# Kernel tuning notes

Hardware: AMD Instinct MI355X
Metric: run time of the kernel (lower is better)

## Reference

```python
import jax, jax.numpy as jnp
import numpy as np

B, E, H, NY, NX = 16, 128, 4, 32, 32


def setup_inputs() -> dict:
    key = jax.random.key(0)
    ks = jax.random.split(key, 7)
    w = lambda k, shape: jax.random.normal(k, shape, jnp.float32) * 0.02
    return {
        "x": jax.random.normal(ks[0], (B, E, NY, NX), jnp.float32),
        "Wk": w(ks[1], (E, E)), "bk": jnp.zeros((E,), jnp.float32),
        "Wq": w(ks[2], (E, E)), "bq": jnp.zeros((E,), jnp.float32),
        "Wv": w(ks[3], (E, E)), "bv": jnp.zeros((E,), jnp.float32),
        "Wu": w(ks[4], (E, E)), "bu": jnp.zeros((E,), jnp.float32),
        "pos_enc": w(ks[5], (H, (2 * NY - 1) * (2 * NX - 1))),
    }


def _conv1x1(x, W, b):
    # 1x1 conv == channel-mixing linear: (B,C,y,x) -> (B,O,y,x)
    return jnp.einsum('bcyx,oc->boyx', x, W) + b[None, :, None, None]


def _rel_indices(ny, nx):
    y = jnp.arange(ny)
    x = jnp.arange(nx)
    y1, x1, y2, x2 = jnp.meshgrid(y, x, y, x, indexing='ij')
    idx = (y1 - y2 + ny - 1) * (2 * nx - 1) + (x1 - x2 + nx - 1)
    return idx.reshape(ny * nx, ny * nx)  # (N, N)


def reference(x, Wk, bk, Wq, bq, Wv, bv, Wu, bu, pos_enc):
    b, e, ny, nx = x.shape
    h = pos_enc.shape[0]
    hc = e // h
    n = ny * nx
    scale = hc ** (-0.5)

    keys = _conv1x1(x, Wk, bk).reshape(b, h, hc, n)
    queries = _conv1x1(x, Wq, bq).reshape(b, h, hc, n)
    values = _conv1x1(x, Wv, bv).reshape(b, h, hc, n)

    # att[b,h,k,q] = sum_c keys[b,h,c,k] * queries[b,h,c,q]
    att = jnp.einsum('bhck,bhcq->bhkq', keys, queries) * scale

    # gathered relative position bias: (H, N, N)
    idx = _rel_indices(ny, nx)
    rel = pos_enc[:, idx]
    att = att + rel[None]

    # softmax over the key axis (dim=-2), as in the original
    att = jax.nn.softmax(att, axis=-2)

    out = jnp.einsum('bhck,bhkq->bhcq', values, att).reshape(b, e, ny, nx)
    return _conv1x1(out, Wu, bu)
```

## Files before the change

kernel.cpp:

```cpp
#include <hip/hip_runtime.h>
#include <hip/hip_bf16.h>

#define BN 16
#define EN 128
#define HN 4
#define HCN 32
#define NN 1024
#define POSN 3969

typedef short short8 __attribute__((ext_vector_type(8)));
typedef float f32x4 __attribute__((ext_vector_type(4)));

#define MFMA16(a, b, c) __builtin_amdgcn_mfma_f32_16x16x32_bf16((a), (b), (c), 0, 0, 0)

union Frag {
  short8 s8;
  uint2 u2[2];
  unsigned int u[4];
  unsigned short us[8];
};

__device__ __forceinline__ unsigned short bfbits(float x) {
  union { __hip_bfloat16 h; unsigned short u; } c;
  c.h = __float2bfloat16(x);
  return c.u;
}

__device__ __forceinline__ unsigned int pk2(float lo, float hi) {
  union { __hip_bfloat162 h2; unsigned int u; } c;
  c.h2 = __float22bfloat162_rn(make_float2(lo, hi));
  return c.u;
}

__device__ __forceinline__ void load_lds16(const void* g, void* l) {
  __builtin_amdgcn_global_load_lds(
      (const __attribute__((address_space(1))) void*)g,
      (__attribute__((address_space(3))) void*)l, 16, 0, 0);
}

__global__ __launch_bounds__(256) void qkv_prep_kernel(
    const float* __restrict__ x,
    const float* __restrict__ Wk, const float* __restrict__ bk, __hip_bfloat16* __restrict__ kb,
    const float* __restrict__ Wq, const float* __restrict__ bq, __hip_bfloat16* __restrict__ qb,
    const float* __restrict__ Wv, const float* __restrict__ bv, __hip_bfloat16* __restrict__ vb,
    const float* __restrict__ Wu, const float* __restrict__ pos,
    unsigned short* __restrict__ bias, Frag* __restrict__ whitab, Frag* __restrict__ wlotab)
{
  const int bid = blockIdx.x, t = threadIdx.x;

  if (bid >= 512) {
    if (bid < 701) {
      const int gid = (bid - 512) * 256 + t;
      const int l = gid & 63;
      const int t2 = gid >> 6;
      const int dxi = t2 % 3;
      const int dy31 = (t2 / 3) % 63;
      const int h = t2 / 189;
      const int rowk0 = (l >> 4) * 4, colq = l & 15;
      const float log2e = 1.4426950408889634f;
      unsigned int bits[4];
#pragma unroll
      for (int j = 0; j < 4; ++j) {
        const int dx = (dxi - 1) * 16 + rowk0 + j - colq + 31;
        bits[j] = (unsigned int)bfbits(pos[h * POSN + dy31 * 63 + dx] * log2e);
      }
      uint2 o;
      o.x = bits[0] | (bits[1] << 16);
      o.y = bits[2] | (bits[3] << 16);
      *(uint2*)(bias + (size_t)gid * 4) = o;
    } else {
      const int fid = (bid - 701) * 256 + t;
      const int ot = fid >> 8, ks = (fid >> 6) & 3, l = fid & 63;
      const int o = ot * 16 + (l & 15), lq = l >> 4;
      const float* wp = Wu + (size_t)o * EN + ks * 32 + lq * 4;
      float4 wa = *(const float4*)wp;
      float4 wb2 = *(const float4*)(wp + 16);
      float v[8] = {wa.x, wa.y, wa.z, wa.w, wb2.x, wb2.y, wb2.z, wb2.w};
      unsigned short hb[8]; float lf[8];
#pragma unroll
      for (int e = 0; e < 8; ++e) {
        __hip_bfloat16 hh = __float2bfloat16(v[e]);
        union { __hip_bfloat16 h; unsigned short u; } c; c.h = hh;
        hb[e] = c.u;
        lf[e] = v[e] - __bfloat162float(hh);
      }
      Frag fh, fl;
#pragma unroll
      for (int e = 0; e < 4; ++e)
        fh.u[e] = hb[2 * e] | ((unsigned int)hb[2 * e + 1] << 16);
      fl.u[0] = pk2(lf[0], lf[1]); fl.u[1] = pk2(lf[2], lf[3]);
      fl.u[2] = pk2(lf[4], lf[5]); fl.u[3] = pk2(lf[6], lf[7]);
      whitab[fid] = fh;
      wlotab[fid] = fl;
    }
    return;
  }

  const int n0 = (bid & 31) * 32;
  const int bb = bid >> 5;
  const int w = t >> 6, l = t & 63;
  const int l15 = l & 15, lq = l >> 4;

  __shared__ unsigned short xs[32][132];

  {
    const float* xb = x + (size_t)bb * EN * NN + n0;
    const int n = t & 31, cg = (t >> 5) * 4;
#pragma unroll
    for (int i = 0; i < 4; ++i) {
      const int cb = cg + i * 32;
      float a0 = xb[(size_t)(cb + 0) * NN + n];
      float a1 = xb[(size_t)(cb + 1) * NN + n];
      float a2 = xb[(size_t)(cb + 2) * NN + n];
      float a3 = xb[(size_t)(cb + 3) * NN + n];
      uint2 v; v.x = pk2(a0, a1); v.y = pk2(a2, a3);
      *(uint2*)&xs[n][cb] = v;
    }
  }
  __syncthreads();

#pragma unroll
  for (int z = 0; z < 3; ++z) {
    const float* W = (z == 0) ? Wk : (z == 1) ? Wq : Wv;
    const float* bias_v = (z == 0) ? bk : (z == 1) ? bq : bv;
    __hip_bfloat16* out = (z == 0) ? kb : (z == 1) ? qb : vb;

    Frag wf[2][4];
#pragma unroll
    for (int r = 0; r < 2; ++r) {
      const int o = (w * 2 + r) * 16 + l15;
#pragma unroll
      for (int ks = 0; ks < 4; ++ks) {
        const float* wp = W + (size_t)o * EN + ks * 32 + lq * 4;
        float4 wa = *(const float4*)wp;
        float4 wb2 = *(const float4*)(wp + 16);
        Frag f;
        f.u[0] = pk2(wa.x, wa.y);   f.u[1] = pk2(wa.z, wa.w);
        f.u[2] = pk2(wb2.x, wb2.y); f.u[3] = pk2(wb2.z, wb2.w);
        wf[r][ks] = f;
      }
    }

    f32x4 acc[2][2];
#pragma unroll
    for (int r = 0; r < 2; ++r)
#pragma unroll
      for (int nt = 0; nt < 2; ++nt) acc[r][nt] = 0.f;

#pragma unroll
    for (int ks = 0; ks < 4; ++ks) {
#pragma unroll
      for (int nt = 0; nt < 2; ++nt) {
        Frag xf;
        xf.u2[0] = *(const uint2*)&xs[nt * 16 + l15][ks * 32 + lq * 4];
        xf.u2[1] = *(const uint2*)&xs[nt * 16 + l15][ks * 32 + lq * 4 + 16];
        if (z < 2) {
          acc[0][nt] = MFMA16(wf[0][ks].s8, xf.s8, acc[0][nt]);
          acc[1][nt] = MFMA16(wf[1][ks].s8, xf.s8, acc[1][nt]);
        } else {
          acc[0][nt] = MFMA16(xf.s8, wf[0][ks].s8, acc[0][nt]);
          acc[1][nt] = MFMA16(xf.s8, wf[1][ks].s8, acc[1][nt]);
        }
      }
    }

    if (z < 2) {
#pragma unroll
      for (int r = 0; r < 2; ++r) {
        const int ob = (w * 2 + r) * 16 + lq * 4;
        const int hh = ob >> 5;
        const int pofs = hh * 32 + ((ob >> 2) & 3) * 8 + ((ob & 16) ? 4 : 0);
        float4 b4 = *(const float4*)(bias_v + ob);
#pragma unroll
        for (int nt = 0; nt < 2; ++nt) {
          const int n = n0 + nt * 16 + l15;
          f32x4 a = acc[r][nt];
          uint2 o2;
          o2.x = pk2(a[0] + b4.x, a[1] + b4.y);
          o2.y = pk2(a[2] + b4.z, a[3] + b4.w);
          *(uint2*)(out + (size_t)(bb * NN + n) * 128 + pofs) = o2;
        }
      }
    } else {
#pragma unroll
      for (int r = 0; r < 2; ++r) {
        const int o = (w * 2 + r) * 16 + l15;
        const int c = o & 31, hh = o >> 5;
        const float bsc = bias_v[o];
#pragma unroll
        for (int nt = 0; nt < 2; ++nt) {
          const int nb = n0 + nt * 16 + lq * 4;
          const int kbk = nb >> 5, k32 = nb & 31;
          const int pofs = ((k32 >> 2) & 3) * 8 + ((k32 & 16) ? 4 : 0);
          f32x4 a = acc[r][nt];
          uint2 o2;
          o2.x = pk2(a[0] + bsc, a[1] + bsc);
          o2.y = pk2(a[2] + bsc, a[3] + bsc);
          *(uint2*)(out + ((size_t)((bb * 4 + hh) * 32 + c) * 32 + kbk) * 32 + pofs) = o2;
        }
      }
    }
  }
}

__global__ __launch_bounds__(256, 4) void attn_mfma_kernel(
    const __hip_bfloat16* __restrict__ kp,
    const __hip_bfloat16* __restrict__ qp,
    const __hip_bfloat16* __restrict__ vp,
    const unsigned short* __restrict__ bias,
    __hip_bfloat16* __restrict__ Opb,
    float* __restrict__ lp)
{
  const int bx = blockIdx.x;
  const int qi = bx & 7, s = bx >> 3;
  const int h = blockIdx.y, b = blockIdx.z;
  const int t = threadIdx.x, w = t >> 6, l = t & 63;
  const int l15 = l & 15, lq = l >> 4;

  __shared__ Frag Kf[2][8][64];
  __shared__ Frag Vf[2][8][64];

  const __hip_bfloat16* kBase = kp + (size_t)b * 131072 + h * 32 + (size_t)l15 * 128 + lq * 8;
  const __hip_bfloat16* vBase = vp + (size_t)((b * 4 + h) * 32 + l15) * 1024 + lq * 8;
  const unsigned short* biasB = bias + (size_t)h * 48384 + l * 4;

#define KADDR(CHG, KT) ((const Frag*)(kBase + (size_t)((CHG) * 128 + (KT) * 16) * 128))
#define VADDR(CHG, SL) ((const Frag*)(vBase + (size_t)((SL) >> 2) * 16384 + ((CHG) * 4 + ((SL) & 3)) * 32))

  const int qt0 = qi * 8 + w * 2;
  Frag qf[2];
  qf[0] = *(const Frag*)(qp + (size_t)(b * 1024 + (qt0 + 0) * 16 + l15) * 128 + h * 32 + lq * 8);
  qf[1] = *(const Frag*)(qp + (size_t)(b * 1024 + (qt0 + 1) * 16 + l15) * 128 + h * 32 + lq * 8);
  const int qy[2] = {(qt0 + 0) >> 1, (qt0 + 1) >> 1};
  const int qx1[2] = {(qt0 + 0) & 1, (qt0 + 1) & 1};

  {
    const int chg = s * 4;
    load_lds16(KADDR(chg, w),     &Kf[0][w][0]);
    load_lds16(KADDR(chg, w + 4), &Kf[0][w + 4][0]);
    load_lds16(VADDR(chg, w),     &Vf[0][w][0]);
    load_lds16(VADDR(chg, w + 4), &Vf[0][w + 4][0]);
  }
  __syncthreads();

  f32x4 O[2][2];
#pragma unroll
  for (int mt = 0; mt < 2; ++mt)
#pragma unroll
    for (int nt = 0; nt < 2; ++nt) O[mt][nt] = 0.f;
  f32x4 Lacc[2]; Lacc[0] = 0.f; Lacc[1] = 0.f;

  Frag ones;
  ones.u[0] = 0x3F803F80u; ones.u[1] = 0x3F803F80u;
  ones.u[2] = 0x3F803F80u; ones.u[3] = 0x3F803F80u;

  const float SCALE2 = 0.17677669529663687f * 1.4426950408889634f;

  for (int c4 = 0; c4 < 4; ++c4) {
    const int buf = c4 & 1;
    const int chg = s * 4 + c4;

    if (c4 < 3) {
      load_lds16(KADDR(chg + 1, w),     &Kf[buf ^ 1][w][0]);
      load_lds16(KADDR(chg + 1, w + 4), &Kf[buf ^ 1][w + 4][0]);
      load_lds16(VADDR(chg + 1, w),     &Vf[buf ^ 1][w][0]);
      load_lds16(VADDR(chg + 1, w + 4), &Vf[buf ^ 1][w + 4][0]);
    }

    uint2 bw[2][2][4];
#pragma unroll
    for (int hh2 = 0; hh2 < 2; ++hh2)
#pragma unroll
      for (int nt = 0; nt < 2; ++nt)
#pragma unroll
        for (int kt = 0; kt < 4; ++kt) {
          const int ktg = chg * 8 + hh2 * 4 + kt;
          const int off = ((ktg >> 1) - qy[nt] + 31) * 768 + ((ktg & 1) - qx1[nt] + 1) * 256;
          bw[hh2][nt][kt] = *(const uint2*)(biasB + off);
        }

#pragma unroll
    for (int hh2 = 0; hh2 < 2; ++hh2) {
      short8 ka[4], va[4];
#pragma unroll
      for (int kt = 0; kt < 4; ++kt) ka[kt] = Kf[buf][hh2 * 4 + kt][l].s8;
#pragma unroll
      for (int mt = 0; mt < 2; ++mt)
#pragma unroll
        for (int kh = 0; kh < 2; ++kh)
          va[mt * 2 + kh] = Vf[buf][mt * 4 + hh2 * 2 + kh][l].s8;

#pragma unroll
      for (int nt = 0; nt < 2; ++nt) {
        __builtin_amdgcn_s_setprio(1);
        f32x4 S[4];
#pragma unroll
        for (int kt = 0; kt < 4; ++kt) {
          f32x4 z = 0.f;
          S[kt] = MFMA16(ka[kt], qf[nt].s8, z);
        }
        __builtin_amdgcn_s_setprio(0);

        Frag B0, B1;
#pragma unroll
        for (int kt = 0; kt < 4; ++kt) {
          const float b0 = __uint_as_float(bw[hh2][nt][kt].x << 16);
          const float b1 = __uint_as_float(bw[hh2][nt][kt].x & 0xffff0000u);
          const float b2 = __uint_as_float(bw[hh2][nt][kt].y << 16);
          const float b3 = __uint_as_float(bw[hh2][nt][kt].y & 0xffff0000u);
          float p0 = exp2f(fmaf(S[kt][0], SCALE2, b0));
          float p1 = exp2f(fmaf(S[kt][1], SCALE2, b1));
          float p2 = exp2f(fmaf(S[kt][2], SCALE2, b2));
          float p3 = exp2f(fmaf(S[kt][3], SCALE2, b3));
          unsigned int lo = pk2(p0, p1), hi = pk2(p2, p3);
          if (kt < 2) { B0.u[kt * 2] = lo; B0.u[kt * 2 + 1] = hi; }
          else        { B1.u[(kt - 2) * 2] = lo; B1.u[(kt - 2) * 2 + 1] = hi; }
        }

        __builtin_amdgcn_s_setprio(1);
        O[0][nt] = MFMA16(va[0], B0.s8, O[0][nt]);
        O[0][nt] = MFMA16(va[1], B1.s8, O[0][nt]);
        O[1][nt] = MFMA16(va[2], B0.s8, O[1][nt]);
        O[1][nt] = MFMA16(va[3], B1.s8, O[1][nt]);
        Lacc[nt] = MFMA16(ones.s8, B0.s8, Lacc[nt]);
        Lacc[nt] = MFMA16(ones.s8, B1.s8, Lacc[nt]);
        __builtin_amdgcn_s_setprio(0);
      }
    }

    if (c4 < 3) __syncthreads();
  }
#undef KADDR
#undef VADDR

  if (lq == 0) {
#pragma unroll
    for (int nt = 0; nt < 2; ++nt)
      lp[((size_t)(s * 16 + b) * 4 + h) * 1024 + (qt0 + nt) * 16 + l15] = Lacc[nt][0];
  }

  __hip_bfloat16* obb = Opb + ((size_t)(s * 16 + b) * 1024) * 128 + h * 32 + lq * 8;
#pragma unroll
  for (int nt = 0; nt < 2; ++nt) {
    const int n = (qt0 + nt) * 16 + l15;
    Frag f;
    f.u[0] = pk2(O[0][nt][0], O[0][nt][1]);
    f.u[1] = pk2(O[0][nt][2], O[0][nt][3]);
    f.u[2] = pk2(O[1][nt][0], O[1][nt][1]);
    f.u[3] = pk2(O[1][nt][2], O[1][nt][3]);
    *(Frag*)(obb + (size_t)n * 128) = f;
  }
}

__global__ __launch_bounds__(256, 2) void conv_final_mfma(
    const __hip_bfloat16* __restrict__ Opb,
    const float* __restrict__ lp,
    const Frag* __restrict__ whitab, const Frag* __restrict__ wlotab,
    const float* __restrict__ bu, float* __restrict__ out)
{
  const int n0 = blockIdx.x * 32;
  const int bb = blockIdx.y;
  const int t = threadIdx.x, w = t >> 6, l = t & 63;
  const int l15 = l & 15, lq = l >> 4;

  __shared__ float rls[4][32];
  if (t < 128) {
    const int h = t >> 5, nl = t & 31;
    const float l0 = lp[((size_t)(0 * 16 + bb) * 4 + h) * 1024 + n0 + nl];
    const float l1 = lp[((size_t)(1 * 16 + bb) * 4 + h) * 1024 + n0 + nl];
    rls[h][nl] = 1.0f / (l0 + l1);
  }

  Frag whi[2][4], wlo[2][4];
#pragma unroll
  for (int r = 0; r < 2; ++r)
#pragma unroll
    for (int ks = 0; ks < 4; ++ks) {
      const int idx = (((w * 2 + r) * 4) + ks) * 64 + l;
      whi[r][ks] = whitab[idx];
      wlo[r][ks] = wlotab[idx];
    }
  __syncthreads();

  f32x4 acc[2][2];
#pragma unroll
  for (int r = 0; r < 2; ++r)
#pragma unroll
    for (int nt = 0; nt < 2; ++nt) acc[r][nt] = 0.f;

#pragma unroll
  for (int s = 0; s < 2; ++s) {
#pragma unroll
    for (int h = 0; h < 4; ++h) {
      Frag a2[2];
#pragma unroll
      for (int nt = 0; nt < 2; ++nt) {
        const int n = n0 + nt * 16 + l15;
        Frag af = *(const Frag*)(Opb + ((size_t)((s * 16 + bb) * 1024 + n)) * 128 + h * 32 + lq * 8);
        const float sc = rls[h][nt * 16 + l15];
        Frag as;
#pragma unroll
        for (int e = 0; e < 4; ++e) {
          const float f0 = __uint_as_float((unsigned int)af.us[2 * e] << 16) * sc;
          const float f1 = __uint_as_float((unsigned int)af.us[2 * e + 1] << 16) * sc;
          as.u[e] = pk2(f0, f1);
        }
        a2[nt] = as;
      }
#pragma unroll
      for (int r = 0; r < 2; ++r)
#pragma unroll
        for (int nt = 0; nt < 2; ++nt) {
          acc[r][nt] = MFMA16(a2[nt].s8, whi[r][h].s8, acc[r][nt]);
          acc[r][nt] = MFMA16(a2[nt].s8, wlo[r][h].s8, acc[r][nt]);
        }
    }
  }

#pragma unroll
  for (int r = 0; r < 2; ++r) {
    const int o = (w * 2 + r) * 16 + l15;
    const float bo = bu[o];
#pragma unroll
    for (int nt = 0; nt < 2; ++nt) {
      const int nb = n0 + nt * 16 + lq * 4;
      f32x4 a = acc[r][nt];
      float4 res = make_float4(a[0] + bo, a[1] + bo, a[2] + bo, a[3] + bo);
      *(float4*)(out + ((size_t)bb * EN + o) * NN + nb) = res;
    }
  }
}

extern "C" void kernel_launch(void* const* d_in, const int* in_sizes, int n_in,
                              void* d_out, int out_size, void* d_ws, size_t ws_size,
                              hipStream_t stream)
{
  const float* x   = (const float*)d_in[0];
  const float* Wk  = (const float*)d_in[1];
  const float* bk  = (const float*)d_in[2];
  const float* Wq  = (const float*)d_in[3];
  const float* bq  = (const float*)d_in[4];
  const float* Wv  = (const float*)d_in[5];
  const float* bv  = (const float*)d_in[6];
  const float* Wu  = (const float*)d_in[7];
  const float* bu  = (const float*)d_in[8];
  const float* pos = (const float*)d_in[9];

  char* ws = (char*)d_ws;
  __hip_bfloat16* kb = (__hip_bfloat16*)(ws);
  __hip_bfloat16* qb = (__hip_bfloat16*)(ws + (size_t)4194304);
  __hip_bfloat16* vb = (__hip_bfloat16*)(ws + (size_t)8388608);
  unsigned short* bias = (unsigned short*)(ws + (size_t)12582912);
  Frag* whitab = (Frag*)(ws + (size_t)13068288);
  Frag* wlotab = (Frag*)(ws + (size_t)13101056);
  float* lp = (float*)(ws + (size_t)13133824);
  __hip_bfloat16* Opb = (__hip_bfloat16*)(ws + (size_t)13658112);

  qkv_prep_kernel<<<709, 256, 0, stream>>>(x, Wk, bk, kb, Wq, bq, qb, Wv, bv, vb,
                                           Wu, pos, bias, whitab, wlotab);

  dim3 g2(16, HN, BN);
  attn_mfma_kernel<<<g2, 256, 0, stream>>>(kb, qb, vb, bias, Opb, lp);

  dim3 g3(32, BN);
  conv_final_mfma<<<g3, 256, 0, stream>>>(Opb, lp, whitab, wlotab, bu, (float*)d_out);
}
```

Measured before the change: 66.76 us.

## Split QKV projection across blocks and replace async LDS loads with register staging

The prep kernel now assigns each of K, Q and V to separate blocks with 64-column tiles, giving 768 projection blocks instead of 512 blocks that each did all three. Weight loading is hoisted before the barrier so it overlaps the x staging. In the attention kernel, the global_load_lds async copies are replaced by loads into registers that are written to the alternate LDS buffer after compute, and bias loads move inside the inner loop to cut register pressure. The trade-off is that x is re-read three times across blocks, and the register-staged prefetch may lengthen the per-chunk critical path or raise register use.

```diff
diff --git a/kernel.cpp b/kernel.cpp
--- a/kernel.cpp
+++ b/kernel.cpp
@@ -32,13 +32,7 @@
   return c.u;
 }
 
-__device__ __forceinline__ void load_lds16(const void* g, void* l) {
-  __builtin_amdgcn_global_load_lds(
-      (const __attribute__((address_space(1))) void*)g,
-      (__attribute__((address_space(3))) void*)l, 16, 0, 0);
-}
-
-__global__ __launch_bounds__(256) void qkv_prep_kernel(
+__global__ __launch_bounds__(256) void conv_prep_kernel(
     const float* __restrict__ x,
     const float* __restrict__ Wk, const float* __restrict__ bk, __hip_bfloat16* __restrict__ kb,
     const float* __restrict__ Wq, const float* __restrict__ bq, __hip_bfloat16* __restrict__ qb,
@@ -48,9 +42,9 @@
 {
   const int bid = blockIdx.x, t = threadIdx.x;
 
-  if (bid >= 512) {
-    if (bid < 701) {
-      const int gid = (bid - 512) * 256 + t;
+  if (bid >= 768) {
+    if (bid < 957) {
+      const int gid = (bid - 768) * 256 + t;
       const int l = gid & 63;
       const int t2 = gid >> 6;
       const int dxi = t2 % 3;
@@ -69,7 +63,7 @@
       o.y = bits[2] | (bits[3] << 16);
       *(uint2*)(bias + (size_t)gid * 4) = o;
     } else {
-      const int fid = (bid - 701) * 256 + t;
+      const int fid = (bid - 957) * 256 + t;
       const int ot = fid >> 8, ks = (fid >> 6) & 3, l = fid & 63;
       const int o = ot * 16 + (l & 15), lq = l >> 4;
       const float* wp = Wu + (size_t)o * EN + ks * 32 + lq * 4;
@@ -96,19 +90,24 @@
     return;
   }
 
-  const int n0 = (bid & 31) * 32;
-  const int bb = bid >> 5;
+  const int z = bid >> 8;
+  const float* W = (z == 0) ? Wk : (z == 1) ? Wq : Wv;
+  const float* bias_v = (z == 0) ? bk : (z == 1) ? bq : bv;
+  __hip_bfloat16* out = (z == 0) ? kb : (z == 1) ? qb : vb;
+
+  const int n0 = (bid & 15) * 64;
+  const int bb = (bid >> 4) & 15;
   const int w = t >> 6, l = t & 63;
   const int l15 = l & 15, lq = l >> 4;
 
-  __shared__ unsigned short xs[32][132];
+  __shared__ unsigned short xs[64][132];
 
   {
     const float* xb = x + (size_t)bb * EN * NN + n0;
-    const int n = t & 31, cg = (t >> 5) * 4;
-#pragma unroll
-    for (int i = 0; i < 4; ++i) {
-      const int cb = cg + i * 32;
+    const int n = t & 63, cg = (t >> 6) * 4;
+#pragma unroll
+    for (int i = 0; i < 8; ++i) {
+      const int cb = cg + i * 16;
       float a0 = xb[(size_t)(cb + 0) * NN + n];
       float a1 = xb[(size_t)(cb + 1) * NN + n];
       float a2 = xb[(size_t)(cb + 2) * NN + n];
@@ -117,87 +116,80 @@
       *(uint2*)&xs[n][cb] = v;
     }
   }
+
+  Frag wf[2][4];
+#pragma unroll
+  for (int r = 0; r < 2; ++r) {
+    const int o = (w * 2 + r) * 16 + l15;
+#pragma unroll
+    for (int ks = 0; ks < 4; ++ks) {
+      const float* wp = W + (size_t)o * EN + ks * 32 + lq * 4;
+      float4 wa = *(const float4*)wp;
+      float4 wb2 = *(const float4*)(wp + 16);
+      Frag f;
+      f.u[0] = pk2(wa.x, wa.y);   f.u[1] = pk2(wa.z, wa.w);
+      f.u[2] = pk2(wb2.x, wb2.y); f.u[3] = pk2(wb2.z, wb2.w);
+      wf[r][ks] = f;
+    }
+  }
   __syncthreads();
 
-#pragma unroll
-  for (int z = 0; z < 3; ++z) {
-    const float* W = (z == 0) ? Wk : (z == 1) ? Wq : Wv;
-    const float* bias_v = (z == 0) ? bk : (z == 1) ? bq : bv;
-    __hip_bfloat16* out = (z == 0) ? kb : (z == 1) ? qb : vb;
-
-    Frag wf[2][4];
+  f32x4 acc[2][4];
+#pragma unroll
+  for (int r = 0; r < 2; ++r)
+#pragma unroll
+    for (int nt = 0; nt < 4; ++nt) acc[r][nt] = 0.f;
+
+#pragma unroll
+  for (int ks = 0; ks < 4; ++ks) {
+#pragma unroll
+    for (int nt = 0; nt < 4; ++nt) {
+      Frag xf;
+      xf.u2[0] = *(const uint2*)&xs[nt * 16 + l15][ks * 32 + lq * 4];
+      xf.u2[1] = *(const uint2*)&xs[nt * 16 + l15][ks * 32 + lq * 4 + 16];
+      if (z < 2) {
+        acc[0][nt] = MFMA16(wf[0][ks].s8, xf.s8, acc[0][nt]);
+        acc[1][nt] = MFMA16(wf[1][ks].s8, xf.s8, acc[1][nt]);
+      } else {
+        acc[0][nt] = MFMA16(xf.s8, wf[0][ks].s8, acc[0][nt]);
+        acc[1][nt] = MFMA16(xf.s8, wf[1][ks].s8, acc[1][nt]);
+      }
+    }
+  }
+
+  if (z < 2) {
+#pragma unroll
+    for (int r = 0; r < 2; ++r) {
+      const int ob = (w * 2 + r) * 16 + lq * 4;
+      const int hh = ob >> 5;
+      const int pofs = hh * 32 + ((ob >> 2) & 3) * 8 + ((ob & 16) ? 4 : 0);
+      float4 b4 = *(const float4*)(bias_v + ob);
+#pragma unroll
+      for (int nt = 0; nt < 4; ++nt) {
+        const int n = n0 + nt * 16 + l15;
+        f32x4 a = acc[r][nt];
+        uint2 o2;
+        o2.x = pk2(a[0] + b4.x, a[1] + b4.y);
+        o2.y = pk2(a[2] + b4.z, a[3] + b4.w);
+        *(uint2*)(out + (size_t)(bb * NN + n) * 128 + pofs) = o2;
+      }
+    }
+  } else {
 #pragma unroll
     for (int r = 0; r < 2; ++r) {
       const int o = (w * 2 + r) * 16 + l15;
-#pragma unroll
-      for (int ks = 0; ks < 4; ++ks) {
-        const float* wp = W + (size_t)o * EN + ks * 32 + lq * 4;
-        float4 wa = *(const float4*)wp;
-        float4 wb2 = *(const float4*)(wp + 16);
-        Frag f;
-        f.u[0] = pk2(wa.x, wa.y);   f.u[1] = pk2(wa.z, wa.w);
-        f.u[2] = pk2(wb2.x, wb2.y); f.u[3] = pk2(wb2.z, wb2.w);
-        wf[r][ks] = f;
-      }
-    }
-
-    f32x4 acc[2][2];
-#pragma unroll
-    for (int r = 0; r < 2; ++r)
-#pragma unroll
-      for (int nt = 0; nt < 2; ++nt) acc[r][nt] = 0.f;
-
-#pragma unroll
-    for (int ks = 0; ks < 4; ++ks) {
-#pragma unroll
-      for (int nt = 0; nt < 2; ++nt) {
-        Frag xf;
-        xf.u2[0] = *(const uint2*)&xs[nt * 16 + l15][ks * 32 + lq * 4];
-        xf.u2[1] = *(const uint2*)&xs[nt * 16 + l15][ks * 32 + lq * 4 + 16];
-        if (z < 2) {
-          acc[0][nt] = MFMA16(wf[0][ks].s8, xf.s8, acc[0][nt]);
-          acc[1][nt] = MFMA16(wf[1][ks].s8, xf.s8, acc[1][nt]);
-        } else {
-          acc[0][nt] = MFMA16(xf.s8, wf[0][ks].s8, acc[0][nt]);
-          acc[1][nt] = MFMA16(xf.s8, wf[1][ks].s8, acc[1][nt]);
-        }
-      }
-    }
-
-    if (z < 2) {
-#pragma unroll
-      for (int r = 0; r < 2; ++r) {
-        const int ob = (w * 2 + r) * 16 + lq * 4;
-        const int hh = ob >> 5;
-        const int pofs = hh * 32 + ((ob >> 2) & 3) * 8 + ((ob & 16) ? 4 : 0);
-        float4 b4 = *(const float4*)(bias_v + ob);
-#pragma unroll
-        for (int nt = 0; nt < 2; ++nt) {
-          const int n = n0 + nt * 16 + l15;
-          f32x4 a = acc[r][nt];
-          uint2 o2;
-          o2.x = pk2(a[0] + b4.x, a[1] + b4.y);
-          o2.y = pk2(a[2] + b4.z, a[3] + b4.w);
-          *(uint2*)(out + (size_t)(bb * NN + n) * 128 + pofs) = o2;
-        }
-      }
-    } else {
-#pragma unroll
-      for (int r = 0; r < 2; ++r) {
-        const int o = (w * 2 + r) * 16 + l15;
-        const int c = o & 31, hh = o >> 5;
-        const float bsc = bias_v[o];
-#pragma unroll
-        for (int nt = 0; nt < 2; ++nt) {
-          const int nb = n0 + nt * 16 + lq * 4;
-          const int kbk = nb >> 5, k32 = nb & 31;
-          const int pofs = ((k32 >> 2) & 3) * 8 + ((k32 & 16) ? 4 : 0);
-          f32x4 a = acc[r][nt];
-          uint2 o2;
-          o2.x = pk2(a[0] + bsc, a[1] + bsc);
-          o2.y = pk2(a[2] + bsc, a[3] + bsc);
-          *(uint2*)(out + ((size_t)((bb * 4 + hh) * 32 + c) * 32 + kbk) * 32 + pofs) = o2;
-        }
+      const int c = o & 31, hh = o >> 5;
+      const float bsc = bias_v[o];
+#pragma unroll
+      for (int nt = 0; nt < 4; ++nt) {
+        const int nb = n0 + nt * 16 + lq * 4;
+        const int kbk = nb >> 5, k32 = nb & 31;
+        const int pofs = ((k32 >> 2) & 3) * 8 + ((k32 & 16) ? 4 : 0);
+        f32x4 a = acc[r][nt];
+        uint2 o2;
+        o2.x = pk2(a[0] + bsc, a[1] + bsc);
+        o2.y = pk2(a[2] + bsc, a[3] + bsc);
+        *(uint2*)(out + ((size_t)((bb * 4 + hh) * 32 + c) * 32 + kbk) * 32 + pofs) = o2;
       }
     }
   }
@@ -236,10 +228,10 @@
 
   {
     const int chg = s * 4;
-    load_lds16(KADDR(chg, w),     &Kf[0][w][0]);
-    load_lds16(KADDR(chg, w + 4), &Kf[0][w + 4][0]);
-    load_lds16(VADDR(chg, w),     &Vf[0][w][0]);
-    load_lds16(VADDR(chg, w + 4), &Vf[0][w + 4][0]);
+    Kf[0][w][l]     = *KADDR(chg, w);
+    Kf[0][w + 4][l] = *KADDR(chg, w + 4);
+    Vf[0][w][l]     = *VADDR(chg, w);
+    Vf[0][w + 4][l] = *VADDR(chg, w + 4);
   }
   __syncthreads();
 
@@ -260,38 +252,35 @@
     const int buf = c4 & 1;
     const int chg = s * 4 + c4;
 
+    Frag kn[2], vn[2];
     if (c4 < 3) {
-      load_lds16(KADDR(chg + 1, w),     &Kf[buf ^ 1][w][0]);
-      load_lds16(KADDR(chg + 1, w + 4), &Kf[buf ^ 1][w + 4][0]);
-      load_lds16(VADDR(chg + 1, w),     &Vf[buf ^ 1][w][0]);
-      load_lds16(VADDR(chg + 1, w + 4), &Vf[buf ^ 1][w + 4][0]);
-    }
-
-    uint2 bw[2][2][4];
-#pragma unroll
-    for (int hh2 = 0; hh2 < 2; ++hh2)
-#pragma unroll
-      for (int nt = 0; nt < 2; ++nt)
+      kn[0] = *KADDR(chg + 1, w);
+      kn[1] = *KADDR(chg + 1, w + 4);
+      vn[0] = *VADDR(chg + 1, w);
+      vn[1] = *VADDR(chg + 1, w + 4);
+    }
+
+#pragma unroll
+    for (int hh2 = 0; hh2 < 2; ++hh2) {
+      short8 ka[4], va[4];
+#pragma unroll
+      for (int kt = 0; kt < 4; ++kt) ka[kt] = Kf[buf][hh2 * 4 + kt][l].s8;
+#pragma unroll
+      for (int mt = 0; mt < 2; ++mt)
+#pragma unroll
+        for (int kh = 0; kh < 2; ++kh)
+          va[mt * 2 + kh] = Vf[buf][mt * 4 + hh2 * 2 + kh][l].s8;
+
+#pragma unroll
+      for (int nt = 0; nt < 2; ++nt) {
+        uint2 bw[4];
 #pragma unroll
         for (int kt = 0; kt < 4; ++kt) {
           const int ktg = chg * 8 + hh2 * 4 + kt;
           const int off = ((ktg >> 1) - qy[nt] + 31) * 768 + ((ktg & 1) - qx1[nt] + 1) * 256;
-          bw[hh2][nt][kt] = *(const uint2*)(biasB + off);
+          bw[kt] = *(const uint2*)(biasB + off);
         }
 
-#pragma unroll
-    for (int hh2 = 0; hh2 < 2; ++hh2) {
-      short8 ka[4], va[4];
-#pragma unroll
-      for (int kt = 0; kt < 4; ++kt) ka[kt] = Kf[buf][hh2 * 4 + kt][l].s8;
-#pragma unroll
-      for (int mt = 0; mt < 2; ++mt)
-#pragma unroll
-        for (int kh = 0; kh < 2; ++kh)
-          va[mt * 2 + kh] = Vf[buf][mt * 4 + hh2 * 2 + kh][l].s8;
-
-#pragma unroll
-      for (int nt = 0; nt < 2; ++nt) {
         __builtin_amdgcn_s_setprio(1);
         f32x4 S[4];
 #pragma unroll
@@ -304,10 +293,10 @@
         Frag B0, B1;
 #pragma unroll
         for (int kt = 0; kt < 4; ++kt) {
-          const float b0 = __uint_as_float(bw[hh2][nt][kt].x << 16);
-          const float b1 = __uint_as_float(bw[hh2][nt][kt].x & 0xffff0000u);
-          const float b2 = __uint_as_float(bw[hh2][nt][kt].y << 16);
-          const float b3 = __uint_as_float(bw[hh2][nt][kt].y & 0xffff0000u);
+          const float b0 = __uint_as_float(bw[kt].x << 16);
+          const float b1 = __uint_as_float(bw[kt].x & 0xffff0000u);
+          const float b2 = __uint_as_float(bw[kt].y << 16);
+          const float b3 = __uint_as_float(bw[kt].y & 0xffff0000u);
           float p0 = exp2f(fmaf(S[kt][0], SCALE2, b0));
           float p1 = exp2f(fmaf(S[kt][1], SCALE2, b1));
           float p2 = exp2f(fmaf(S[kt][2], SCALE2, b2));
@@ -328,7 +317,13 @@
       }
     }
 
-    if (c4 < 3) __syncthreads();
+    if (c4 < 3) {
+      Kf[buf ^ 1][w][l]     = kn[0];
+      Kf[buf ^ 1][w + 4][l] = kn[1];
+      Vf[buf ^ 1][w][l]     = vn[0];
+      Vf[buf ^ 1][w + 4][l] = vn[1];
+      __syncthreads();
+    }
   }
 #undef KADDR
 #undef VADDR
@@ -456,8 +451,8 @@
   float* lp = (float*)(ws + (size_t)13133824);
   __hip_bfloat16* Opb = (__hip_bfloat16*)(ws + (size_t)13658112);
 
-  qkv_prep_kernel<<<709, 256, 0, stream>>>(x, Wk, bk, kb, Wq, bq, qb, Wv, bv, vb,
-                                           Wu, pos, bias, whitab, wlotab);
+  conv_prep_kernel<<<965, 256, 0, stream>>>(x, Wk, bk, kb, Wq, bq, qb, Wv, bv, vb,
+                                            Wu, pos, bias, whitab, wlotab);
 
   dim3 g2(16, HN, BN);
   attn_mfma_kernel<<<g2, 256, 0, stream>>>(kb, qb, vb, bias, Opb, lp);
```

After: 57.42 us. 14.0% less time.
